# Performance work log

Measured on AMD Instinct MI355X. Metric: run time of the kernel, lower is better.

## Reference

```python
import jax, jax.numpy as jnp
import numpy as np

N_NODES = 50000
N_EDGES = 800000
H_DIM = 64
N_RELS = 8
N_BASES = 2
N_LAYERS = 2


def setup_inputs() -> dict:
    key = jax.random.key(0)
    ks = jax.random.split(key, 10)
    scale = 1.0 / np.sqrt(H_DIM)
    features = jax.random.normal(ks[0], (N_NODES, H_DIM), dtype=jnp.float32)
    src = jax.random.randint(ks[1], (N_EDGES,), 0, N_NODES, dtype=jnp.int32)
    dst = jax.random.randint(ks[2], (N_EDGES,), 0, N_NODES, dtype=jnp.int32)
    etype = jax.random.randint(ks[3], (N_EDGES,), 0, N_RELS, dtype=jnp.int32)
    # basis weights V: [L, B, H, H], coefficients comp: [L, R, B]
    V = jax.random.normal(ks[4], (N_LAYERS, N_BASES, H_DIM, H_DIM), dtype=jnp.float32) * scale
    comp = jax.random.normal(ks[5], (N_LAYERS, N_RELS, N_BASES), dtype=jnp.float32)
    loop_w = jax.random.normal(ks[6], (N_LAYERS, H_DIM, H_DIM), dtype=jnp.float32) * scale
    layer_bias = jnp.zeros((N_LAYERS, H_DIM), dtype=jnp.float32)
    fc_w = jax.random.normal(ks[7], (1, N_NODES * H_DIM), dtype=jnp.float32) * (1.0 / np.sqrt(N_NODES * H_DIM))
    fc_b = jnp.zeros((1,), dtype=jnp.float32)
    return {
        "features": features, "V": V, "comp": comp, "loop_w": loop_w,
        "layer_bias": layer_bias, "fc_w": fc_w, "fc_b": fc_b,
        "src": src, "dst": dst, "etype": etype,
    }


def reference(features, V, comp, loop_w, layer_bias, fc_w, fc_b, src, dst, etype):
    N, H = features.shape
    L = V.shape[0]
    x = features
    for l in range(L):
        # basis decomposition: project nodes through each basis first (N*B*H, cheap),
        # then mix per-edge with relation coefficients -> avoids per-edge [H,H] weights
        proj = jnp.einsum('ni,bio->nbo', x, V[l])          # [N, B, H]
        msg = jnp.einsum('eb,ebo->eo', comp[l][etype], proj[src])  # [E, H]
        agg = jax.ops.segment_sum(msg, dst, num_segments=N)        # [N, H]
        h = agg + x @ loop_w[l] + layer_bias[l]
        x = jax.nn.relu(h) if l < L - 1 else h
    flat = x.reshape(1, -1)                                # [1, N*H]
    return jax.nn.sigmoid(flat @ fc_w.T + fc_b)            # [1, 1]
```

## Files before the change

### kernel.cpp

```cpp
#include <hip/hip_runtime.h>
#include <hip/hip_bf16.h>
#include <math.h>

#define N_NODES 50000
#define N_EDGES 800000
#define HDIM 64

#define NBUCKET 98
#define BSHIFT  9
#define BCAP    10240

typedef short bf16x8 __attribute__((ext_vector_type(8)));
typedef float f32x4  __attribute__((ext_vector_type(4)));
typedef unsigned short ushort_t;

__device__ __forceinline__ ushort_t f2bf(float f) {
    __hip_bfloat16 b = __float2bfloat16(f);
    return *(ushort_t*)&b;
}
__device__ __forceinline__ void unpack8(uint4 u, float* f) {
    f[0] = __uint_as_float(u.x << 16); f[1] = __uint_as_float(u.x & 0xFFFF0000u);
    f[2] = __uint_as_float(u.y << 16); f[3] = __uint_as_float(u.y & 0xFFFF0000u);
    f[4] = __uint_as_float(u.z << 16); f[5] = __uint_as_float(u.z & 0xFFFF0000u);
    f[6] = __uint_as_float(u.w << 16); f[7] = __uint_as_float(u.w & 0xFFFF0000u);
}

__global__ __launch_bounds__(256) void prep_kernel(
    const float* __restrict__ features, ushort_t* __restrict__ x_bf,
    const float* __restrict__ V, const float* __restrict__ lw,
    ushort_t* __restrict__ Wt, int* __restrict__ bucketFill,
    float* __restrict__ scalar, int* __restrict__ done)
{
    const int b = blockIdx.x;
    const int t = threadIdx.x;
    if (b < 3125) {
        const int i = b * 256 + t;
        const float4 v = ((const float4*)features)[i];
        ushort4 o = { f2bf(v.x), f2bf(v.y), f2bf(v.z), f2bf(v.w) };
        *(ushort4*)&x_bf[(size_t)i * 4] = o;
    } else if (b < 3221) {
        const int e = (b - 3125) * 256 + t;
        const int l = e / 12288, r = e % 12288;
        const int n = r / 192, k = r % 192;
        const int sel = k >> 6, i = k & 63;
        const float val = (sel < 2) ? V[l * 8192 + sel * 4096 + i * 64 + n]
                                    : lw[l * 4096 + i * 64 + n];
        Wt[e] = f2bf(val);
    } else {
        if (t < NBUCKET) bucketFill[t] = 0;
        if (t == NBUCKET) scalar[0] = 0.0f;
        if (t == NBUCKET + 1) done[0] = 0;
    }
}

__global__ __launch_bounds__(256) void bucket_scatter(
    const int* __restrict__ src, const int* __restrict__ dst,
    const int* __restrict__ etype, int* __restrict__ bucketFill,
    unsigned int* __restrict__ buf)
{
    __shared__ int cnt[NBUCKET];
    __shared__ int base[NBUCKET];
    const int t = threadIdx.x;
    if (t < NBUCKET) cnt[t] = 0;
    __syncthreads();

    int rank[8], bkt[8];
    unsigned pay[8];
    bool valid[8];
#pragma unroll
    for (int k = 0; k < 8; ++k) {
        const int e = blockIdx.x * 2048 + k * 256 + t;
        valid[k] = (e < N_EDGES);
        if (valid[k]) {
            const int d = dst[e];
            const int b = d >> BSHIFT;
            bkt[k] = b;
            pay[k] = (unsigned)src[e] | ((unsigned)etype[e] << 16)
                   | ((unsigned)(d & 511) << 19);
            rank[k] = atomicAdd(&cnt[b], 1);
        }
    }
    __syncthreads();
    if (t < NBUCKET) base[t] = atomicAdd(&bucketFill[t], cnt[t]);
    __syncthreads();
#pragma unroll
    for (int k = 0; k < 8; ++k) {
        if (valid[k]) {
            const int pos = base[bkt[k]] + rank[k];
            if (pos < BCAP) buf[bkt[k] * BCAP + pos] = pay[k];
        }
    }
}

__global__ __launch_bounds__(256) void bucket_sort(
    const unsigned int* __restrict__ buf, const int* __restrict__ bucketFill,
    unsigned int* __restrict__ edges, int* __restrict__ row_ptr)
{
    __shared__ int hist[512];
    __shared__ int lscan[512];
    __shared__ int cnt2[512];
    __shared__ int sfill[128];
    __shared__ int sbase;
    const int b = blockIdx.x;
    const int t = threadIdx.x;

    hist[t] = 0; hist[t + 256] = 0;
    cnt2[t] = 0; cnt2[t + 256] = 0;
    if (t < NBUCKET) sfill[t] = bucketFill[t];
    else if (t < 128) sfill[t] = 0;
    __syncthreads();

    for (int off = 1; off < 128; off <<= 1) {
        int u = (t >= off && t < 128) ? sfill[t - off] : 0;
        __syncthreads();
        if (t < 128) sfill[t] += u;
        __syncthreads();
    }
    const int cntb = min(bucketFill[b], BCAP);
    if (t == 0) sbase = sfill[b] - bucketFill[b];
    __syncthreads();
    const int bb = sbase;

    for (int i = t; i < cntb; i += 256)
        atomicAdd(&hist[buf[b * BCAP + i] >> 19], 1);
    __syncthreads();

    if (t < 64) {
        int carry = 0;
        for (int c = 0; c < 8; ++c) {
            const int h = hist[c * 64 + t];
            int x = h;
#pragma unroll
            for (int off = 1; off < 64; off <<= 1) {
                int u = __shfl_up(x, off, 64);
                if (t >= off) x += u;
            }
            lscan[c * 64 + t] = carry + x - h;
            carry += __shfl(x, 63, 64);
        }
    }
    __syncthreads();

    const int n0 = b << BSHIFT;
    for (int i = t; i < 512; i += 256) {
        const int g = n0 + i;
        if (g < N_NODES) row_ptr[g] = bb + lscan[i];
    }
    if (b == NBUCKET - 1 && t == 0) row_ptr[N_NODES] = bb + cntb;

    for (int i = t; i < cntb; i += 256) {
        const unsigned p = buf[b * BCAP + i];
        const int d = p >> 19;
        const int r = atomicAdd(&cnt2[d], 1);
        edges[bb + lscan[d] + r] = p & 0x7FFFFu;
    }
}

__global__ __launch_bounds__(256) void aggregate_bf(
    const ushort_t* __restrict__ x,
    const unsigned int* __restrict__ edges,
    const int* __restrict__ row_ptr,
    const float* __restrict__ comp_l,
    ushort_t* __restrict__ y)
{
    const int lane = threadIdx.x & 63;
    const int wv   = threadIdx.x >> 6;
    const int fo   = lane & 7;
    const int g    = lane >> 3;
    const int n    = blockIdx.x * 32 + wv * 8 + g;

    int beg = 0, end = 0;
    if (n < N_NODES) { beg = row_ptr[n]; end = row_ptr[n + 1]; }

    float a0[8], a1[8];
#pragma unroll
    for (int i = 0; i < 8; ++i) { a0[i] = 0.f; a1[i] = 0.f; }

    for (int j = beg; j < end; j += 4) {
        unsigned pk[4];
        float2 c[4];
#pragma unroll
        for (int k = 0; k < 4; ++k) {
            const int jk = j + k;
            const unsigned p = edges[(jk < end) ? jk : (end - 1)];
            pk[k] = p;
            float2 cc = *(const float2*)&comp_l[(p >> 16) * 2];
            if (jk >= end) { cc.x = 0.f; cc.y = 0.f; }
            c[k] = cc;
        }
        uint4 u[4];
#pragma unroll
        for (int k = 0; k < 4; ++k)
            u[k] = *(const uint4*)&x[(size_t)(pk[k] & 0xFFFFu) * 64 + fo * 8];
#pragma unroll
        for (int k = 0; k < 4; ++k) {
            float f[8];
            unpack8(u[k], f);
#pragma unroll
            for (int i = 0; i < 8; ++i) {
                a0[i] = fmaf(c[k].x, f[i], a0[i]);
                a1[i] = fmaf(c[k].y, f[i], a1[i]);
            }
        }
    }

    if (n < N_NODES) {
        uint4 o0, o1;
        o0.x = (unsigned)f2bf(a0[0]) | ((unsigned)f2bf(a0[1]) << 16);
        o0.y = (unsigned)f2bf(a0[2]) | ((unsigned)f2bf(a0[3]) << 16);
        o0.z = (unsigned)f2bf(a0[4]) | ((unsigned)f2bf(a0[5]) << 16);
        o0.w = (unsigned)f2bf(a0[6]) | ((unsigned)f2bf(a0[7]) << 16);
        o1.x = (unsigned)f2bf(a1[0]) | ((unsigned)f2bf(a1[1]) << 16);
        o1.y = (unsigned)f2bf(a1[2]) | ((unsigned)f2bf(a1[3]) << 16);
        o1.z = (unsigned)f2bf(a1[4]) | ((unsigned)f2bf(a1[5]) << 16);
        o1.w = (unsigned)f2bf(a1[6]) | ((unsigned)f2bf(a1[7]) << 16);
        *(uint4*)&y[(size_t)n * 128 + fo * 8]      = o0;
        *(uint4*)&y[(size_t)n * 128 + 64 + fo * 8] = o1;
    }
}

template <bool FUSE>
__global__ __launch_bounds__(256) void mfma_transform(
    const ushort_t* __restrict__ y_bf,
    const ushort_t* __restrict__ x_bf,
    const ushort_t* __restrict__ Wt,
    const float* __restrict__ bias,
    const float* __restrict__ fcw,
    ushort_t* __restrict__ xout,
    float* __restrict__ scalar,
    const float* __restrict__ fcb,
    int* __restrict__ done,
    float* __restrict__ outp)
{
    __shared__ __align__(16) ushort_t su[64 * 200];
    __shared__ float sred[4];
    const int t = threadIdx.x;
    const int w = t >> 6;
    const int lane = t & 63;
    const int c16 = lane & 15;
    const int quad = lane >> 4;
    const int tile = blockIdx.x;

    bf16x8 wf[6];
#pragma unroll
    for (int kf = 0; kf < 6; ++kf)
        wf[kf] = *(const bf16x8*)&Wt[(w * 16 + c16) * 192 + kf * 32 + quad * 8];
    const float bv = bias[w * 16 + c16];

#pragma unroll
    for (int k = 0; k < 6; ++k) {
        const int cid = t + 256 * k;
        const int row = cid / 24;
        const int part = cid % 24;
        const int n = tile * 64 + row;
        uint4 v = {0u, 0u, 0u, 0u};
        if (n < N_NODES) {
            v = (part < 16) ? *(const uint4*)&y_bf[(size_t)n * 128 + part * 8]
                            : *(const uint4*)&x_bf[(size_t)n * 64 + (part - 16) * 8];
        }
        *(uint4*)&su[row * 200 + part * 8] = v;
    }
    __syncthreads();

    float fsum = 0.f;
#pragma unroll
    for (int mt = 0; mt < 4; ++mt) {
        f32x4 acc = {bv, bv, bv, bv};
#pragma unroll
        for (int kf = 0; kf < 6; ++kf) {
            const bf16x8 af =
                *(const bf16x8*)&su[(mt * 16 + c16) * 200 + kf * 32 + quad * 8];
            acc = __builtin_amdgcn_mfma_f32_16x16x32_bf16(af, wf[kf], acc, 0, 0, 0);
        }
        const int nodeb = tile * 64 + mt * 16 + quad * 4;
        if (FUSE) {
#pragma unroll
            for (int r = 0; r < 4; ++r) {
                const int n = nodeb + r;
                if (n < N_NODES)
                    fsum += acc[r] * fcw[(size_t)n * 64 + w * 16 + c16];
            }
        } else {
#pragma unroll
            for (int r = 0; r < 4; ++r) {
                const int n = nodeb + r;
                if (n < N_NODES)
                    xout[(size_t)n * 64 + w * 16 + c16] = f2bf(fmaxf(acc[r], 0.f));
            }
        }
    }

    if (FUSE) {
#pragma unroll
        for (int off = 32; off; off >>= 1) fsum += __shfl_down(fsum, off, 64);
        if (lane == 0) sred[w] = fsum;
        __syncthreads();
        if (t == 0) {
            atomicAdd(scalar, sred[0] + sred[1] + sred[2] + sred[3]);
            __threadfence();
            const int ticket = atomicAdd(done, 1);
            if (ticket == (int)gridDim.x - 1) {
                const float v = atomicAdd(scalar, 0.0f) + fcb[0];
                outp[0] = 1.0f / (1.0f + expf(-v));
            }
        }
    }
}

extern "C" void kernel_launch(void* const* d_in, const int* in_sizes, int n_in,
                              void* d_out, int out_size, void* d_ws, size_t ws_size,
                              hipStream_t stream)
{
    const float* features = (const float*)d_in[0];
    const float* V        = (const float*)d_in[1];
    const float* comp     = (const float*)d_in[2];
    const float* loop_w   = (const float*)d_in[3];
    const float* bias     = (const float*)d_in[4];
    const float* fc_w     = (const float*)d_in[5];
    const float* fc_b     = (const float*)d_in[6];
    const int*   src      = (const int*)d_in[7];
    const int*   dst      = (const int*)d_in[8];
    const int*   etype    = (const int*)d_in[9];
    float* out = (float*)d_out;

    char* ws = (char*)d_ws;
    ushort_t*     y_bf    = (ushort_t*)(ws);
    ushort_t*     x_bf    = (ushort_t*)(ws + 12800000);
    ushort_t*     x1_bf   = (ushort_t*)(ws + 19200000);
    ushort_t*     Wt      = (ushort_t*)(ws + 25600000);
    float*        scalar  = (float*)   (ws + 25649152);
    int*          done    = (int*)     (ws + 25649160);
    int*          bucketFill = (int*)  (ws + 25649280);
    int*          row_ptr = (int*)     (ws + 25649792);
    unsigned int* edges   = (unsigned int*)(ws + 25849856);
    unsigned int* buf     = (unsigned int*)(ws + 29049856);

    const int aggBlocks = (N_NODES + 31) / 32;
    const int mtBlocks  = (N_NODES + 63) / 64;
    const int k1Blocks  = (N_EDGES + 2047) / 2048;

    prep_kernel<<<3222, 256, 0, stream>>>(features, x_bf, V, loop_w, Wt,
                                          bucketFill, scalar, done);
    bucket_scatter<<<k1Blocks, 256, 0, stream>>>(src, dst, etype, bucketFill, buf);
    bucket_sort<<<NBUCKET, 256, 0, stream>>>(buf, bucketFill, edges, row_ptr);

    aggregate_bf<<<aggBlocks, 256, 0, stream>>>(x_bf, edges, row_ptr, comp, y_bf);
    mfma_transform<false><<<mtBlocks, 256, 0, stream>>>(
        y_bf, x_bf, Wt, bias, nullptr, x1_bf, nullptr, nullptr, nullptr, nullptr);

    aggregate_bf<<<aggBlocks, 256, 0, stream>>>(x1_bf, edges, row_ptr, comp + 16, y_bf);
    mfma_transform<true><<<mtBlocks, 256, 0, stream>>>(
        y_bf, x1_bf, Wt + 12288, bias + 64, fc_w, nullptr, scalar, fc_b, done, out);
}
```

Baseline: 199.9 us.

## Fuse aggregation with MFMA transform and use finer dst buckets for sorting

Merges the per-node edge aggregation and the MFMA weight transform into one kernel per layer, so the aggregated bf16 messages stay in shared memory instead of round-tripping through a global y buffer. Each block now handles 32 nodes, which halves the MFMA tile. The bucket sort moves from 98 buckets of 512 nodes to 392 buckets of 128 nodes, which gives more sort blocks, a smaller per-block histogram and a 4-way unrolled load loop. The trade-off is fewer MFMA tiles per block and a lower per-bucket capacity of 3072, which could overflow if the degree distribution is skewed.

```diff
diff --git a/kernel.cpp b/kernel.cpp
--- a/kernel.cpp
+++ b/kernel.cpp
@@ -6,9 +6,10 @@
 #define N_EDGES 800000
 #define HDIM 64
 
-#define NBUCKET 98
-#define BSHIFT  9
-#define BCAP    10240
+#define NBUCKET 392
+#define BSHIFT  7
+#define NLOC    128
+#define BCAP    3072
 
 typedef short bf16x8 __attribute__((ext_vector_type(8)));
 typedef float f32x4  __attribute__((ext_vector_type(4)));
@@ -47,9 +48,8 @@
                                     : lw[l * 4096 + i * 64 + n];
         Wt[e] = f2bf(val);
     } else {
-        if (t < NBUCKET) bucketFill[t] = 0;
-        if (t == NBUCKET) scalar[0] = 0.0f;
-        if (t == NBUCKET + 1) done[0] = 0;
+        for (int i = t; i < NBUCKET; i += 256) bucketFill[i] = 0;
+        if (t == 0) { scalar[0] = 0.0f; done[0] = 0; }
     }
 }
 
@@ -61,7 +61,7 @@
     __shared__ int cnt[NBUCKET];
     __shared__ int base[NBUCKET];
     const int t = threadIdx.x;
-    if (t < NBUCKET) cnt[t] = 0;
+    for (int i = t; i < NBUCKET; i += 256) cnt[i] = 0;
     __syncthreads();
 
     int rank[8], bkt[8];
@@ -76,12 +76,13 @@
             const int b = d >> BSHIFT;
             bkt[k] = b;
             pay[k] = (unsigned)src[e] | ((unsigned)etype[e] << 16)
-                   | ((unsigned)(d & 511) << 19);
+                   | ((unsigned)(d & (NLOC - 1)) << 19);
             rank[k] = atomicAdd(&cnt[b], 1);
         }
     }
     __syncthreads();
-    if (t < NBUCKET) base[t] = atomicAdd(&bucketFill[t], cnt[t]);
+    for (int i = t; i < NBUCKET; i += 256)
+        base[i] = atomicAdd(&bucketFill[i], cnt[i]);
     __syncthreads();
 #pragma unroll
     for (int k = 0; k < 8; ++k) {
@@ -96,45 +97,61 @@
     const unsigned int* __restrict__ buf, const int* __restrict__ bucketFill,
     unsigned int* __restrict__ edges, int* __restrict__ row_ptr)
 {
-    __shared__ int hist[512];
-    __shared__ int lscan[512];
-    __shared__ int cnt2[512];
-    __shared__ int sfill[128];
-    __shared__ int sbase;
+    __shared__ int hist[NLOC];
+    __shared__ int lscan[NLOC];
+    __shared__ int cnt2[NLOC];
+    __shared__ int sraw[448];
+    __shared__ int sexc[448];
     const int b = blockIdx.x;
     const int t = threadIdx.x;
 
-    hist[t] = 0; hist[t + 256] = 0;
-    cnt2[t] = 0; cnt2[t + 256] = 0;
-    if (t < NBUCKET) sfill[t] = bucketFill[t];
-    else if (t < 128) sfill[t] = 0;
-    __syncthreads();
-
-    for (int off = 1; off < 128; off <<= 1) {
-        int u = (t >= off && t < 128) ? sfill[t - off] : 0;
-        __syncthreads();
-        if (t < 128) sfill[t] += u;
-        __syncthreads();
-    }
-    const int cntb = min(bucketFill[b], BCAP);
-    if (t == 0) sbase = sfill[b] - bucketFill[b];
-    __syncthreads();
-    const int bb = sbase;
-
-    for (int i = t; i < cntb; i += 256)
-        atomicAdd(&hist[buf[b * BCAP + i] >> 19], 1);
+    if (t < NLOC) { hist[t] = 0; cnt2[t] = 0; }
+    for (int i = t; i < 448; i += 256)
+        sraw[i] = (i < NBUCKET) ? bucketFill[i] : 0;
     __syncthreads();
 
     if (t < 64) {
         int carry = 0;
-        for (int c = 0; c < 8; ++c) {
-            const int h = hist[c * 64 + t];
+        for (int c = 0; c < 7; ++c) {
+            const int h = sraw[c * 64 + t];
             int x = h;
 #pragma unroll
             for (int off = 1; off < 64; off <<= 1) {
                 int u = __shfl_up(x, off, 64);
                 if (t >= off) x += u;
             }
+            sexc[c * 64 + t] = carry + x - h;
+            carry += __shfl(x, 63, 64);
+        }
+    }
+    __syncthreads();
+    const int cntb = min(sraw[b], BCAP);
+    const int bb   = sexc[b];
+
+    for (int i0 = t; i0 < cntb; i0 += 1024) {
+        const bool v1 = i0 + 256 < cntb, v2 = i0 + 512 < cntb, v3 = i0 + 768 < cntb;
+        const unsigned p0 = buf[b * BCAP + i0];
+        unsigned p1 = 0, p2 = 0, p3 = 0;
+        if (v1) p1 = buf[b * BCAP + i0 + 256];
+        if (v2) p2 = buf[b * BCAP + i0 + 512];
+        if (v3) p3 = buf[b * BCAP + i0 + 768];
+        atomicAdd(&hist[p0 >> 19], 1);
+        if (v1) atomicAdd(&hist[p1 >> 19], 1);
+        if (v2) atomicAdd(&hist[p2 >> 19], 1);
+        if (v3) atomicAdd(&hist[p3 >> 19], 1);
+    }
+    __syncthreads();
+
+    if (t < 64) {
+        int carry = 0;
+        for (int c = 0; c < 2; ++c) {
+            const int h = hist[c * 64 + t];
+            int x = h;
+#pragma unroll
+            for (int off = 1; off < 64; off <<= 1) {
+                int u = __shfl_up(x, off, 64);
+                if (t >= off) x += u;
+            }
             lscan[c * 64 + t] = carry + x - h;
             carry += __shfl(x, 63, 64);
         }
@@ -142,87 +159,39 @@
     __syncthreads();
 
     const int n0 = b << BSHIFT;
-    for (int i = t; i < 512; i += 256) {
-        const int g = n0 + i;
-        if (g < N_NODES) row_ptr[g] = bb + lscan[i];
+    if (t < NLOC) {
+        const int g = n0 + t;
+        if (g < N_NODES) row_ptr[g] = bb + lscan[t];
     }
     if (b == NBUCKET - 1 && t == 0) row_ptr[N_NODES] = bb + cntb;
 
-    for (int i = t; i < cntb; i += 256) {
-        const unsigned p = buf[b * BCAP + i];
-        const int d = p >> 19;
-        const int r = atomicAdd(&cnt2[d], 1);
-        edges[bb + lscan[d] + r] = p & 0x7FFFFu;
-    }
-}
-
-__global__ __launch_bounds__(256) void aggregate_bf(
-    const ushort_t* __restrict__ x,
+    for (int i0 = t; i0 < cntb; i0 += 1024) {
+        const bool v1 = i0 + 256 < cntb, v2 = i0 + 512 < cntb, v3 = i0 + 768 < cntb;
+        const unsigned p0 = buf[b * BCAP + i0];
+        unsigned p1 = 0, p2 = 0, p3 = 0;
+        if (v1) p1 = buf[b * BCAP + i0 + 256];
+        if (v2) p2 = buf[b * BCAP + i0 + 512];
+        if (v3) p3 = buf[b * BCAP + i0 + 768];
+        {
+            const int d = p0 >> 19;
+            const int r = atomicAdd(&cnt2[d], 1);
+            edges[bb + lscan[d] + r] = p0 & 0x7FFFFu;
+        }
+        if (v1) { const int d = p1 >> 19; const int r = atomicAdd(&cnt2[d], 1);
+                  edges[bb + lscan[d] + r] = p1 & 0x7FFFFu; }
+        if (v2) { const int d = p2 >> 19; const int r = atomicAdd(&cnt2[d], 1);
+                  edges[bb + lscan[d] + r] = p2 & 0x7FFFFu; }
+        if (v3) { const int d = p3 >> 19; const int r = atomicAdd(&cnt2[d], 1);
+                  edges[bb + lscan[d] + r] = p3 & 0x7FFFFu; }
+    }
+}
+
+template <bool FUSE>
+__global__ __launch_bounds__(256) void fused_layer(
+    const ushort_t* __restrict__ xin,
     const unsigned int* __restrict__ edges,
     const int* __restrict__ row_ptr,
     const float* __restrict__ comp_l,
-    ushort_t* __restrict__ y)
-{
-    const int lane = threadIdx.x & 63;
-    const int wv   = threadIdx.x >> 6;
-    const int fo   = lane & 7;
-    const int g    = lane >> 3;
-    const int n    = blockIdx.x * 32 + wv * 8 + g;
-
-    int beg = 0, end = 0;
-    if (n < N_NODES) { beg = row_ptr[n]; end = row_ptr[n + 1]; }
-
-    float a0[8], a1[8];
-#pragma unroll
-    for (int i = 0; i < 8; ++i) { a0[i] = 0.f; a1[i] = 0.f; }
-
-    for (int j = beg; j < end; j += 4) {
-        unsigned pk[4];
-        float2 c[4];
-#pragma unroll
-        for (int k = 0; k < 4; ++k) {
-            const int jk = j + k;
-            const unsigned p = edges[(jk < end) ? jk : (end - 1)];
-            pk[k] = p;
-            float2 cc = *(const float2*)&comp_l[(p >> 16) * 2];
-            if (jk >= end) { cc.x = 0.f; cc.y = 0.f; }
-            c[k] = cc;
-        }
-        uint4 u[4];
-#pragma unroll
-        for (int k = 0; k < 4; ++k)
-            u[k] = *(const uint4*)&x[(size_t)(pk[k] & 0xFFFFu) * 64 + fo * 8];
-#pragma unroll
-        for (int k = 0; k < 4; ++k) {
-            float f[8];
-            unpack8(u[k], f);
-#pragma unroll
-            for (int i = 0; i < 8; ++i) {
-                a0[i] = fmaf(c[k].x, f[i], a0[i]);
-                a1[i] = fmaf(c[k].y, f[i], a1[i]);
-            }
-        }
-    }
-
-    if (n < N_NODES) {
-        uint4 o0, o1;
-        o0.x = (unsigned)f2bf(a0[0]) | ((unsigned)f2bf(a0[1]) << 16);
-        o0.y = (unsigned)f2bf(a0[2]) | ((unsigned)f2bf(a0[3]) << 16);
-        o0.z = (unsigned)f2bf(a0[4]) | ((unsigned)f2bf(a0[5]) << 16);
-        o0.w = (unsigned)f2bf(a0[6]) | ((unsigned)f2bf(a0[7]) << 16);
-        o1.x = (unsigned)f2bf(a1[0]) | ((unsigned)f2bf(a1[1]) << 16);
-        o1.y = (unsigned)f2bf(a1[2]) | ((unsigned)f2bf(a1[3]) << 16);
-        o1.z = (unsigned)f2bf(a1[4]) | ((unsigned)f2bf(a1[5]) << 16);
-        o1.w = (unsigned)f2bf(a1[6]) | ((unsigned)f2bf(a1[7]) << 16);
-        *(uint4*)&y[(size_t)n * 128 + fo * 8]      = o0;
-        *(uint4*)&y[(size_t)n * 128 + 64 + fo * 8] = o1;
-    }
-}
-
-template <bool FUSE>
-__global__ __launch_bounds__(256) void mfma_transform(
-    const ushort_t* __restrict__ y_bf,
-    const ushort_t* __restrict__ x_bf,
     const ushort_t* __restrict__ Wt,
     const float* __restrict__ bias,
     const float* __restrict__ fcw,
@@ -232,14 +201,70 @@
     int* __restrict__ done,
     float* __restrict__ outp)
 {
-    __shared__ __align__(16) ushort_t su[64 * 200];
+    __shared__ __align__(16) ushort_t su[32 * 200];
     __shared__ float sred[4];
     const int t = threadIdx.x;
-    const int w = t >> 6;
+    const int tile = blockIdx.x;
+
+    const int grp = t >> 3;
+    const int fo  = t & 7;
+    const int n   = tile * 32 + grp;
+
+    int beg = 0, end = 0;
+    if (n < N_NODES) { beg = row_ptr[n]; end = row_ptr[n + 1]; }
+
+    float a0[8], a1[8];
+#pragma unroll
+    for (int i = 0; i < 8; ++i) { a0[i] = 0.f; a1[i] = 0.f; }
+
+    for (int j = beg; j < end; j += 4) {
+        unsigned pk[4];
+        float2 c[4];
+#pragma unroll
+        for (int k = 0; k < 4; ++k) {
+            const int jk = j + k;
+            const unsigned p = edges[(jk < end) ? jk : (end - 1)];
+            pk[k] = p;
+            float2 cc = *(const float2*)&comp_l[(p >> 16) * 2];
+            if (jk >= end) { cc.x = 0.f; cc.y = 0.f; }
+            c[k] = cc;
+        }
+        uint4 u[4];
+#pragma unroll
+        for (int k = 0; k < 4; ++k)
+            u[k] = *(const uint4*)&xin[(size_t)(pk[k] & 0xFFFFu) * 64 + fo * 8];
+#pragma unroll
+        for (int k = 0; k < 4; ++k) {
+            float f[8];
+            unpack8(u[k], f);
+#pragma unroll
+            for (int i = 0; i < 8; ++i) {
+                a0[i] = fmaf(c[k].x, f[i], a0[i]);
+                a1[i] = fmaf(c[k].y, f[i], a1[i]);
+            }
+        }
+    }
+
+    uint4 o0, o1;
+    o0.x = (unsigned)f2bf(a0[0]) | ((unsigned)f2bf(a0[1]) << 16);
+    o0.y = (unsigned)f2bf(a0[2]) | ((unsigned)f2bf(a0[3]) << 16);
+    o0.z = (unsigned)f2bf(a0[4]) | ((unsigned)f2bf(a0[5]) << 16);
+    o0.w = (unsigned)f2bf(a0[6]) | ((unsigned)f2bf(a0[7]) << 16);
+    o1.x = (unsigned)f2bf(a1[0]) | ((unsigned)f2bf(a1[1]) << 16);
+    o1.y = (unsigned)f2bf(a1[2]) | ((unsigned)f2bf(a1[3]) << 16);
+    o1.z = (unsigned)f2bf(a1[4]) | ((unsigned)f2bf(a1[5]) << 16);
+    o1.w = (unsigned)f2bf(a1[6]) | ((unsigned)f2bf(a1[7]) << 16);
+    uint4 xt = {0u, 0u, 0u, 0u};
+    if (n < N_NODES) xt = *(const uint4*)&xin[(size_t)n * 64 + fo * 8];
+    *(uint4*)&su[grp * 200 + fo * 8]        = o0;
+    *(uint4*)&su[grp * 200 + (8 + fo) * 8]  = o1;
+    *(uint4*)&su[grp * 200 + (16 + fo) * 8] = xt;
+    __syncthreads();
+
+    const int w    = t >> 6;
     const int lane = t & 63;
-    const int c16 = lane & 15;
+    const int c16  = lane & 15;
     const int quad = lane >> 4;
-    const int tile = blockIdx.x;
 
     bf16x8 wf[6];
 #pragma unroll
@@ -247,24 +272,9 @@
         wf[kf] = *(const bf16x8*)&Wt[(w * 16 + c16) * 192 + kf * 32 + quad * 8];
     const float bv = bias[w * 16 + c16];
 
-#pragma unroll
-    for (int k = 0; k < 6; ++k) {
-        const int cid = t + 256 * k;
-        const int row = cid / 24;
-        const int part = cid % 24;
-        const int n = tile * 64 + row;
-        uint4 v = {0u, 0u, 0u, 0u};
-        if (n < N_NODES) {
-            v = (part < 16) ? *(const uint4*)&y_bf[(size_t)n * 128 + part * 8]
-                            : *(const uint4*)&x_bf[(size_t)n * 64 + (part - 16) * 8];
-        }
-        *(uint4*)&su[row * 200 + part * 8] = v;
-    }
-    __syncthreads();
-
     float fsum = 0.f;
 #pragma unroll
-    for (int mt = 0; mt < 4; ++mt) {
+    for (int mt = 0; mt < 2; ++mt) {
         f32x4 acc = {bv, bv, bv, bv};
 #pragma unroll
         for (int kf = 0; kf < 6; ++kf) {
@@ -272,20 +282,20 @@
                 *(const bf16x8*)&su[(mt * 16 + c16) * 200 + kf * 32 + quad * 8];
             acc = __builtin_amdgcn_mfma_f32_16x16x32_bf16(af, wf[kf], acc, 0, 0, 0);
         }
-        const int nodeb = tile * 64 + mt * 16 + quad * 4;
+        const int nodeb = tile * 32 + mt * 16 + quad * 4;
         if (FUSE) {
 #pragma unroll
             for (int r = 0; r < 4; ++r) {
-                const int n = nodeb + r;
-                if (n < N_NODES)
-                    fsum += acc[r] * fcw[(size_t)n * 64 + w * 16 + c16];
+                const int nn = nodeb + r;
+                if (nn < N_NODES)
+                    fsum += acc[r] * fcw[(size_t)nn * 64 + w * 16 + c16];
             }
         } else {
 #pragma unroll
             for (int r = 0; r < 4; ++r) {
-                const int n = nodeb + r;
-                if (n < N_NODES)
-                    xout[(size_t)n * 64 + w * 16 + c16] = f2bf(fmaxf(acc[r], 0.f));
+                const int nn = nodeb + r;
+                if (nn < N_NODES)
+                    xout[(size_t)nn * 64 + w * 16 + c16] = f2bf(fmaxf(acc[r], 0.f));
             }
         }
     }
@@ -324,31 +334,29 @@
     float* out = (float*)d_out;
 
     char* ws = (char*)d_ws;
-    ushort_t*     y_bf    = (ushort_t*)(ws);
-    ushort_t*     x_bf    = (ushort_t*)(ws + 12800000);
-    ushort_t*     x1_bf   = (ushort_t*)(ws + 19200000);
-    ushort_t*     Wt      = (ushort_t*)(ws + 25600000);
-    float*        scalar  = (float*)   (ws + 25649152);
-    int*          done    = (int*)     (ws + 25649160);
-    int*          bucketFill = (int*)  (ws + 25649280);
-    int*          row_ptr = (int*)     (ws + 25649792);
-    unsigned int* edges   = (unsigned int*)(ws + 25849856);
-    unsigned int* buf     = (unsigned int*)(ws + 29049856);
-
-    const int aggBlocks = (N_NODES + 31) / 32;
-    const int mtBlocks  = (N_NODES + 63) / 64;
-    const int k1Blocks  = (N_EDGES + 2047) / 2048;
+    ushort_t*     x_bf    = (ushort_t*)(ws);
+    ushort_t*     x1_bf   = (ushort_t*)(ws + 6400000);
+    ushort_t*     Wt      = (ushort_t*)(ws + 12800000);
+    float*        scalar  = (float*)   (ws + 12849152);
+    int*          done    = (int*)     (ws + 12849156);
+    int*          bucketFill = (int*)  (ws + 12849280);
+    int*          row_ptr = (int*)     (ws + 12850944);
+    unsigned int* edges   = (unsigned int*)(ws + 13051008);
+    unsigned int* buf     = (unsigned int*)(ws + 16251008);
+
+    const int flBlocks = (N_NODES + 31) / 32;
+    const int k1Blocks = (N_EDGES + 2047) / 2048;
 
     prep_kernel<<<3222, 256, 0, stream>>>(features, x_bf, V, loop_w, Wt,
                                           bucketFill, scalar, done);
     bucket_scatter<<<k1Blocks, 256, 0, stream>>>(src, dst, etype, bucketFill, buf);
     bucket_sort<<<NBUCKET, 256, 0, stream>>>(buf, bucketFill, edges, row_ptr);
 
-    aggregate_bf<<<aggBlocks, 256, 0, stream>>>(x_bf, edges, row_ptr, comp, y_bf);
-    mfma_transform<false><<<mtBlocks, 256, 0, stream>>>(
-        y_bf, x_bf, Wt, bias, nullptr, x1_bf, nullptr, nullptr, nullptr, nullptr);
-
-    aggregate_bf<<<aggBlocks, 256, 0, stream>>>(x1_bf, edges, row_ptr, comp + 16, y_bf);
-    mfma_transform<true><<<mtBlocks, 256, 0, stream>>>(
-        y_bf, x1_bf, Wt + 12288, bias + 64, fc_w, nullptr, scalar, fc_b, done, out);
-}
+    fused_layer<false><<<flBlocks, 256, 0, stream>>>(
+        x_bf, edges, row_ptr, comp, Wt, bias, nullptr, x1_bf,
+        nullptr, nullptr, nullptr, nullptr);
+
+    fused_layer<true><<<flBlocks, 256, 0, stream>>>(
+        x1_bf, edges, row_ptr, comp + 16, Wt + 12288, bias + 64, fc_w, nullptr,
+        scalar, fc_b, done, out);
+}
```

New measurement: 206.3 us. 1.03x slower.
